# Performance work log

Measured on AMD Instinct MI355X. Metric: run time of the kernel, lower is better.

Reference implementation:

```python
import jax, jax.numpy as jnp
import numpy as np

SEQ_LEN = 12
EMB = 64        # embedding_dim
H = 128         # dec_h_dim
MLP = 1024      # mlp_dim
Z = 32          # z_dim
ZX = MLP + Z    # 1056, width of cat([enc_h_feat, z])
B = 32768


def setup_inputs() -> dict:
    key = jax.random.key(0)
    ks = jax.random.split(key, 16)
    s = 0.05  # weight scale to keep the recurrence stable
    return {
        "last_pos": jax.random.normal(ks[0], (B, 2), jnp.float32),
        "last_pos_rel": jax.random.normal(ks[1], (B, 2), jnp.float32),
        "enc_h_feat": jax.random.normal(ks[2], (B, MLP), jnp.float32),
        "z": jax.random.normal(ks[3], (B, Z), jnp.float32),
        "seq_start_end": jnp.zeros((1, 2), jnp.int64),
        # LSTM params (PyTorch layout: gates ordered i,f,g,o along rows)
        "W_ih": jax.random.normal(ks[4], (4 * H, ZX + EMB), jnp.float32) * s,
        "W_hh": jax.random.normal(ks[5], (4 * H, H), jnp.float32) * s,
        "b_ih": jax.random.normal(ks[6], (4 * H,), jnp.float32) * s,
        "b_hh": jax.random.normal(ks[7], (4 * H,), jnp.float32) * s,
        # mlp: Linear(ZX->MLP), ReLU, Linear(MLP->H), ReLU
        "W1": jax.random.normal(ks[8], (MLP, ZX), jnp.float32) * s,
        "b1": jax.random.normal(ks[9], (MLP,), jnp.float32) * s,
        "W2": jax.random.normal(ks[10], (H, MLP), jnp.float32) * s,
        "b2": jax.random.normal(ks[11], (H,), jnp.float32) * s,
        # spatial_embedding: Linear(2 -> EMB)
        "W_sp": jax.random.normal(ks[12], (EMB, 2), jnp.float32) * s,
        "b_sp": jax.random.normal(ks[13], (EMB,), jnp.float32) * s,
        # hidden2pos: Linear(H -> 2)
        "W_hp": jax.random.normal(ks[14], (2, H), jnp.float32) * s,
        "b_hp": jax.random.normal(ks[15], (2,), jnp.float32) * s,
    }


def _decode(last_pos, last_pos_rel, enc_h_feat, z,
            W_ih, W_hh, b_ih, b_hh, W1, b1, W2, b2, W_sp, b_sp, W_hp, b_hp):
    # initial decoder input from last relative position
    dec_inp = last_pos_rel @ W_sp.T + b_sp                     # [B, EMB]
    zx = jnp.concatenate([enc_h_feat, z], axis=1)              # [B, ZX]
    h = jax.nn.relu(jax.nn.relu(zx @ W1.T + b1) @ W2.T + b2)   # [B, H]
    c = jnp.zeros_like(h)
    # zx is constant across steps: precompute its gate contribution + biases
    W_zx, W_emb = W_ih[:, :ZX], W_ih[:, ZX:]
    zx_proj = zx @ W_zx.T + b_ih + b_hh                        # [B, 4H]

    def step(carry, _):
        h, c, last_pos, dec_inp = carry
        gates = zx_proj + dec_inp @ W_emb.T + h @ W_hh.T       # [B, 4H]
        i, f, g, o = jnp.split(gates, 4, axis=1)
        c = jax.nn.sigmoid(f) * c + jax.nn.sigmoid(i) * jnp.tanh(g)
        h = jax.nn.sigmoid(o) * jnp.tanh(c)
        rel_pos = h @ W_hp.T + b_hp                            # [B, 2]
        last_pos = rel_pos + last_pos
        dec_inp = rel_pos @ W_sp.T + b_sp
        return (h, c, last_pos, dec_inp), rel_pos

    _, pred = jax.lax.scan(step, (h, c, last_pos, dec_inp), None, length=SEQ_LEN)
    return pred  # [SEQ_LEN, B, 2]


def reference(last_pos, last_pos_rel, enc_h_feat, z, seq_start_end,
              W_ih, W_hh, b_ih, b_hh, W1, b1, W2, b2, W_sp, b_sp, W_hp, b_hp):
    # seq_start_end is unused by the original forward
    return _decode(last_pos, last_pos_rel, enc_h_feat, z,
                   W_ih, W_hh, b_ih, b_hh, W1, b1, W2, b2, W_sp, b_sp, W_hp, b_hp)
```

## Files before the change

kernel.cpp:

```cpp
#include <hip/hip_runtime.h>

#define BATCH   32768
#define SEQLEN  12
#define EMB     64
#define H       128
#define MLP     1024
#define Z       32
#define ZX      1056
#define KP      1088
#define NG      512

typedef _Float16 f16x8 __attribute__((ext_vector_type(8)));
typedef float    f32x4 __attribute__((ext_vector_type(4)));

#define S_WCAT_OFF   0u
#define S_W2H_OFF    3244032u
#define S_WHHF_OFF   3506176u
#define S_WC_OFF     3637248u
#define S_BIAS2_OFF  3641344u
#define S_T1_OFF     3643392u
#define S_GP_OFF     70752256u
#define S_H0_OFF     137861120u
#define B_WCAT_OFF   0u
#define B_W2H_OFF    3342336u
#define B_WHHF_OFF   3604480u
#define B_WC_OFF     3735552u
#define B_BIAS2_OFF  3739648u
#define B_T1_OFF     3741696u
#define B_GP_OFF     70850560u
#define B_H0_OFF     137959424u
#define B_ZX16_OFF   146348032u
#define B_TOTAL      217651200ull

__device__ __forceinline__ float sigf(float x) {
    return __builtin_amdgcn_rcpf(1.0f + __expf(-x));
}
__device__ __forceinline__ float tanhfast(float x) {
    return 2.0f * __builtin_amdgcn_rcpf(1.0f + __expf(-2.0f * x)) - 1.0f;
}

__device__ __forceinline__ void gload16(const void* g, void* l) {
    __builtin_amdgcn_global_load_lds(
        (const __attribute__((address_space(1))) unsigned int*)(unsigned long long)(uintptr_t)g,
        (__attribute__((address_space(3))) unsigned int*)(unsigned int)(uintptr_t)l,
        16, 0, 0);
}

__global__ __launch_bounds__(256) void prep_kernel(
    const float* __restrict__ W_ih, const float* __restrict__ W_hh_in,
    const float* __restrict__ b_ih, const float* __restrict__ b_hh,
    const float* __restrict__ W1,   const float* __restrict__ W2,
    const float* __restrict__ W_sp, const float* __restrict__ b_sp,
    const float* __restrict__ W_hp, int cs,
    _Float16* __restrict__ wcat, _Float16* __restrict__ w2h,
    _Float16* __restrict__ whhf, float* __restrict__ wc, float* __restrict__ bias2)
{
    const int bid = blockIdx.x;
    const int tid = threadIdx.x;
    if (bid < 1536) {
        const float* src = (bid < 1024) ? (W1 + (size_t)bid * ZX)
                                        : (W_ih + (size_t)(bid - 1024) * 1120);
        _Float16* dst = wcat + (size_t)bid * cs;
        for (int k = tid; k < cs; k += 256)
            dst[k] = (k < ZX) ? (_Float16)src[k] : (_Float16)0.f;
    } else if (bid < 1664) {
        const int n = bid - 1536;
        for (int k = tid; k < MLP; k += 256)
            w2h[n * MLP + k] = (_Float16)W2[n * MLP + k];
    } else if (bid < 1920) {
        const int n = (bid - 1664) * 2 + (tid >> 7);
        const int k = tid & 127;
        float wc0 = 0.f, wc1 = 0.f;
        for (int e = 0; e < EMB; ++e) {
            const float we = W_ih[(size_t)n * 1120 + ZX + e];
            wc0 += we * W_sp[e * 2];
            wc1 += we * W_sp[e * 2 + 1];
        }
        whhf[n * H + k] = (_Float16)(W_hh_in[n * H + k] + wc0 * W_hp[k] + wc1 * W_hp[H + k]);
    } else {
        const int t = (bid - 1920) * 256 + tid;
        if (t < 1024) {
            const int n = t >> 1, j = t & 1;
            float s = 0.f;
            for (int e = 0; e < EMB; ++e)
                s += W_ih[(size_t)n * 1120 + ZX + e] * W_sp[e * 2 + j];
            wc[t] = s;
        } else if (t < 1536) {
            const int n = t - 1024;
            float s = b_ih[n] + b_hh[n];
            for (int e = 0; e < EMB; ++e)
                s += W_ih[(size_t)n * 1120 + ZX + e] * b_sp[e];
            bias2[n] = s;
        }
    }
}

__global__ __launch_bounds__(256) void zxcast_kernel(
    const float* __restrict__ enc, const float* __restrict__ zin,
    _Float16* __restrict__ zx16)
{
    const int gid = blockIdx.x * 256 + threadIdx.x;
    if (gid < 4194304) {
        const int row = gid >> 7, cw = gid & 127;
        const float4* s = (const float4*)(enc + (size_t)row * MLP + cw * 8);
        const float4 f0 = s[0], f1 = s[1];
        f16x8 v = {(_Float16)f0.x, (_Float16)f0.y, (_Float16)f0.z, (_Float16)f0.w,
                   (_Float16)f1.x, (_Float16)f1.y, (_Float16)f1.z, (_Float16)f1.w};
        *(f16x8*)(zx16 + (size_t)row * KP + cw * 8) = v;
    } else if (gid < 4325376) {
        const int g2 = gid - 4194304;
        const int row = g2 >> 2, cw = g2 & 3;
        const float4* s = (const float4*)(zin + (size_t)row * Z + cw * 8);
        const float4 f0 = s[0], f1 = s[1];
        f16x8 v = {(_Float16)f0.x, (_Float16)f0.y, (_Float16)f0.z, (_Float16)f0.w,
                   (_Float16)f1.x, (_Float16)f1.y, (_Float16)f1.z, (_Float16)f1.w};
        *(f16x8*)(zx16 + (size_t)row * KP + MLP + cw * 8) = v;
    } else {
        const int g2 = gid - 4325376;
        const int row = g2 >> 2, cw = g2 & 3;
        f16x8 v = {};
        *(f16x8*)(zx16 + (size_t)row * KP + ZX + cw * 8) = v;
    }
}

__global__ __launch_bounds__(512, 2) void gemm1_big_kernel(
    const _Float16* __restrict__ zx16, const _Float16* __restrict__ wcat,
    const float* __restrict__ bias1, const float* __restrict__ bias2g,
    _Float16* __restrict__ t1, float* __restrict__ gperm)
{
    __shared__ _Float16 s_a[2][256 * 64];
    __shared__ _Float16 s_b[2][256 * 64];

    const int tid = threadIdx.x;
    const int b   = blockIdx.x;
    const int swz = (b & 7) * 96 + (b >> 3);
    const int mt  = swz / 6, nt = swz % 6;
    const int m0  = mt * 256, n0 = nt * 256;

    const int lane = tid & 63, wv = tid >> 6;
    const int wm   = wv >> 2,  wn = wv & 3;
    const int l15  = lane & 15, q = lane >> 4;

    const int rowS = tid >> 3;
    const int chS  = (tid & 7) ^ (rowS & 7);

    const _Float16* gA = zx16 + (size_t)(m0 + rowS) * KP + chS * 8;
    const _Float16* gB = wcat + (size_t)(n0 + rowS) * KP + chS * 8;
    const size_t rstep = (size_t)64 * KP;

    const int ph0  = q ^ (l15 & 7);
    const int ph1  = (4 + q) ^ (l15 & 7);
    const int aof0 = (wm * 128 + l15) * 64 + ph0 * 8;
    const int aof1 = (wm * 128 + l15) * 64 + ph1 * 8;
    const int bof0 = (wn * 64 + l15) * 64 + ph0 * 8;
    const int bof1 = (wn * 64 + l15) * 64 + ph1 * 8;

    f32x4 acc[8][4] = {};

    {
        _Float16* dA = &s_a[0][0] + wv * 512;
        _Float16* dB = &s_b[0][0] + wv * 512;
        #pragma unroll
        for (int j = 0; j < 4; ++j) gload16(gA + j * rstep, dA + j * 4096);
        #pragma unroll
        for (int j = 0; j < 4; ++j) gload16(gB + j * rstep, dB + j * 4096);
    }

    #pragma unroll 2
    for (int kt = 0; kt < 16; ++kt) {
        const int cur = kt & 1;
        const _Float16* sA = &s_a[cur][0];
        const _Float16* sB = &s_b[cur][0];
        _Float16* dA = &s_a[cur ^ 1][0] + wv * 512;
        _Float16* dB = &s_b[cur ^ 1][0] + wv * 512;
        const _Float16* gA1 = gA + (kt + 1) * 64;
        const _Float16* gB1 = gB + (kt + 1) * 64;

        f16x8 af[4], bf[4];

        gload16(gA1,         dA);
        gload16(gA1 + rstep, dA + 4096);
        asm volatile("s_waitcnt vmcnt(2)\n\ts_barrier" ::: "memory");
        #pragma unroll
        for (int i = 0; i < 4; ++i) af[i] = *(const f16x8*)(sA + aof0 + i * 1024);
        #pragma unroll
        for (int i = 0; i < 4; ++i) bf[i] = *(const f16x8*)(sB + bof0 + i * 1024);
        __builtin_amdgcn_s_setprio(1);
        #pragma unroll
        for (int n_ = 0; n_ < 4; ++n_)
            #pragma unroll
            for (int m_ = 0; m_ < 4; ++m_)
                acc[m_][n_] = __builtin_amdgcn_mfma_f32_16x16x32_f16(af[m_], bf[n_], acc[m_][n_], 0, 0, 0);
        __builtin_amdgcn_s_setprio(0);
        asm volatile("s_barrier" ::: "memory");

        gload16(gA1 + 2 * rstep, dA + 8192);
        gload16(gA1 + 3 * rstep, dA + 12288);
        #pragma unroll
        for (int i = 0; i < 4; ++i) af[i] = *(const f16x8*)(sA + aof0 + 4096 + i * 1024);
        asm volatile("s_barrier" ::: "memory");
        __builtin_amdgcn_s_setprio(1);
        #pragma unroll
        for (int n_ = 0; n_ < 4; ++n_)
            #pragma unroll
            for (int m_ = 0; m_ < 4; ++m_)
                acc[4 + m_][n_] = __builtin_amdgcn_mfma_f32_16x16x32_f16(af[m_], bf[n_], acc[4 + m_][n_], 0, 0, 0);
        __builtin_amdgcn_s_setprio(0);
        asm volatile("s_barrier" ::: "memory");

        gload16(gB1,         dB);
        gload16(gB1 + rstep, dB + 4096);
        #pragma unroll
        for (int i = 0; i < 4; ++i) af[i] = *(const f16x8*)(sA + aof1 + i * 1024);
        #pragma unroll
        for (int i = 0; i < 4; ++i) bf[i] = *(const f16x8*)(sB + bof1 + i * 1024);
        asm volatile("s_barrier" ::: "memory");
        __builtin_amdgcn_s_setprio(1);
        #pragma unroll
        for (int n_ = 0; n_ < 4; ++n_)
            #pragma unroll
            for (int m_ = 0; m_ < 4; ++m_)
                acc[m_][n_] = __builtin_amdgcn_mfma_f32_16x16x32_f16(af[m_], bf[n_], acc[m_][n_], 0, 0, 0);
        __builtin_amdgcn_s_setprio(0);
        asm volatile("s_barrier" ::: "memory");

        gload16(gB1 + 2 * rstep, dB + 8192);
        gload16(gB1 + 3 * rstep, dB + 12288);
        #pragma unroll
        for (int i = 0; i < 4; ++i) af[i] = *(const f16x8*)(sA + aof1 + 4096 + i * 1024);
        asm volatile("s_barrier" ::: "memory");
        __builtin_amdgcn_s_setprio(1);
        #pragma unroll
        for (int n_ = 0; n_ < 4; ++n_)
            #pragma unroll
            for (int m_ = 0; m_ < 4; ++m_)
                acc[4 + m_][n_] = __builtin_amdgcn_mfma_f32_16x16x32_f16(af[m_], bf[n_], acc[4 + m_][n_], 0, 0, 0);
        __builtin_amdgcn_s_setprio(0);
        asm volatile("s_barrier" ::: "memory");
    }

    {
        const _Float16* sA = &s_a[0][0];
        const _Float16* sB = &s_b[0][0];
        asm volatile("s_waitcnt vmcnt(0)\n\ts_barrier" ::: "memory");
        f16x8 af[4], bf[4];
        #pragma unroll
        for (int i = 0; i < 4; ++i) af[i] = *(const f16x8*)(sA + aof0 + i * 1024);
        #pragma unroll
        for (int i = 0; i < 4; ++i) bf[i] = *(const f16x8*)(sB + bof0 + i * 1024);
        __builtin_amdgcn_s_setprio(1);
        #pragma unroll
        for (int n_ = 0; n_ < 4; ++n_)
            #pragma unroll
            for (int m_ = 0; m_ < 4; ++m_)
                acc[m_][n_] = __builtin_amdgcn_mfma_f32_16x16x32_f16(af[m_], bf[n_], acc[m_][n_], 0, 0, 0);
        #pragma unroll
        for (int i = 0; i < 4; ++i) af[i] = *(const f16x8*)(sA + aof0 + 4096 + i * 1024);
        #pragma unroll
        for (int n_ = 0; n_ < 4; ++n_)
            #pragma unroll
            for (int m_ = 0; m_ < 4; ++m_)
                acc[4 + m_][n_] = __builtin_amdgcn_mfma_f32_16x16x32_f16(af[m_], bf[n_], acc[4 + m_][n_], 0, 0, 0);
        #pragma unroll
        for (int i = 0; i < 4; ++i) af[i] = *(const f16x8*)(sA + aof1 + i * 1024);
        #pragma unroll
        for (int i = 0; i < 4; ++i) bf[i] = *(const f16x8*)(sB + bof1 + i * 1024);
        #pragma unroll
        for (int n_ = 0; n_ < 4; ++n_)
            #pragma unroll
            for (int m_ = 0; m_ < 4; ++m_)
                acc[m_][n_] = __builtin_amdgcn_mfma_f32_16x16x32_f16(af[m_], bf[n_], acc[m_][n_], 0, 0, 0);
        #pragma unroll
        for (int i = 0; i < 4; ++i) af[i] = *(const f16x8*)(sA + aof1 + 4096 + i * 1024);
        #pragma unroll
        for (int n_ = 0; n_ < 4; ++n_)
            #pragma unroll
            for (int m_ = 0; m_ < 4; ++m_)
                acc[4 + m_][n_] = __builtin_amdgcn_mfma_f32_16x16x32_f16(af[m_], bf[n_], acc[4 + m_][n_], 0, 0, 0);
        __builtin_amdgcn_s_setprio(0);
    }

    if (nt < 4) {
        #pragma unroll
        for (int im = 0; im < 8; ++im)
            #pragma unroll
            for (int in_ = 0; in_ < 4; ++in_) {
                const int n = n0 + wn * 64 + in_ * 16 + l15;
                const float bb = bias1[n];
                const int mbase = m0 + wm * 128 + im * 16 + q * 4;
                #pragma unroll
                for (int r = 0; r < 4; ++r) {
                    float v = acc[im][in_][r] + bb;
                    v = v > 0.f ? v : 0.f;
                    t1[(size_t)(mbase + r) * MLP + n] = (_Float16)v;
                }
            }
    } else {
        #pragma unroll
        for (int im = 0; im < 8; ++im)
            #pragma unroll
            for (int in_ = 0; in_ < 4; ++in_) {
                const int n = (n0 - 1024) + wn * 64 + in_ * 16 + l15;
                const float bb = bias2g[n];
                const int m4 = (m0 + wm * 128 + im * 16 + q * 4) >> 2;
                float4 v;
                v.x = acc[im][in_][0] + bb;
                v.y = acc[im][in_][1] + bb;
                v.z = acc[im][in_][2] + bb;
                v.w = acc[im][in_][3] + bb;
                *(float4*)(gperm + ((size_t)m4 * NG + n) * 4) = v;
            }
    }
}

__global__ __launch_bounds__(256) void gemm1_small_kernel(
    const float* __restrict__ enc, const float* __restrict__ zin,
    const _Float16* __restrict__ wcat,
    const float* __restrict__ bias1, const float* __restrict__ bias2g,
    _Float16* __restrict__ t1, float* __restrict__ gperm)
{
    __shared__ float    s_a[128 * 32];
    __shared__ _Float16 s_b[128 * 32];

    const int tid = threadIdx.x;
    const int b = blockIdx.x;
    const int x = b & 7, s = b >> 3;
    const int mt = x * 32 + s / 12;
    const int bn = s % 12;
    const int m0 = mt * 128;

    const int lane = tid & 63, wv = tid >> 6;
    const int wm = wv >> 1, wn = wv & 1;
    const int l15 = lane & 15, q = lane >> 4;

    const int rowA = tid >> 3;
    const int chA  = (tid & 7) ^ ((tid >> 3) & 7);
    const int rowB = tid >> 2;
    const int chB  = (tid & 3) ^ ((tid >> 3) & 3);

    const int ca0 = (2 * q) ^ (l15 & 7);
    const int cb  = q ^ ((l15 >> 1) & 3);

    f32x4 acc[4][4] = {};

    for (int kt = 0; kt < 33; ++kt) {
        const float* abase;
        size_t astride;
        if (kt < 32) { abase = enc + (size_t)m0 * MLP + kt * 32; astride = MLP; }
        else         { abase = zin + (size_t)m0 * Z;             astride = Z;   }

        __syncthreads();
        #pragma unroll
        for (int i = 0; i < 4; ++i)
            gload16(abase + (size_t)(i * 32 + rowA) * astride + chA * 4,
                    s_a + i * 1024 + wv * 256);
        #pragma unroll
        for (int i = 0; i < 2; ++i)
            gload16(wcat + (size_t)(bn * 128 + i * 64 + rowB) * ZX + kt * 32 + chB * 8,
                    s_b + i * 2048 + wv * 512);
        __syncthreads();

        f16x8 af[4];
        #pragma unroll
        for (int im = 0; im < 4; ++im) {
            const float* ap = s_a + (wm * 64 + im * 16 + l15) * 32;
            const float4 f0 = *(const float4*)(ap + ca0 * 4);
            const float4 f1 = *(const float4*)(ap + (ca0 ^ 1) * 4);
            af[im] = f16x8{(_Float16)f0.x, (_Float16)f0.y, (_Float16)f0.z, (_Float16)f0.w,
                           (_Float16)f1.x, (_Float16)f1.y, (_Float16)f1.z, (_Float16)f1.w};
        }
        #pragma unroll
        for (int in_ = 0; in_ < 4; ++in_) {
            const f16x8 bf = *(const f16x8*)(s_b + (wn * 64 + in_ * 16 + l15) * 32 + cb * 8);
            #pragma unroll
            for (int im = 0; im < 4; ++im)
                acc[im][in_] = __builtin_amdgcn_mfma_f32_16x16x32_f16(af[im], bf, acc[im][in_], 0, 0, 0);
        }
    }

    if (bn < 8) {
        #pragma unroll
        for (int im = 0; im < 4; ++im)
            #pragma unroll
            for (int in_ = 0; in_ < 4; ++in_) {
                const int n = bn * 128 + wn * 64 + in_ * 16 + l15;
                const float bb = bias1[n];
                #pragma unroll
                for (int r = 0; r < 4; ++r) {
                    const int m = m0 + wm * 64 + im * 16 + q * 4 + r;
                    float v = acc[im][in_][r] + bb;
                    v = v > 0.f ? v : 0.f;
                    t1[(size_t)m * MLP + n] = (_Float16)v;
                }
            }
    } else {
        #pragma unroll
        for (int im = 0; im < 4; ++im)
            #pragma unroll
            for (int in_ = 0; in_ < 4; ++in_) {
                const int n = (bn - 8) * 128 + wn * 64 + in_ * 16 + l15;
                const float bb = bias2g[n];
                const int m4 = (m0 + wm * 64 + im * 16 + q * 4) >> 2;
                float4 v;
                v.x = acc[im][in_][0] + bb;
                v.y = acc[im][in_][1] + bb;
                v.z = acc[im][in_][2] + bb;
                v.w = acc[im][in_][3] + bb;
                *(float4*)(gperm + ((size_t)m4 * NG + n) * 4) = v;
            }
    }
}

__global__ __launch_bounds__(256) void gemm2_kernel(
    const _Float16* __restrict__ t1, const _Float16* __restrict__ w2h,
    const float* __restrict__ b2, _Float16* __restrict__ h0buf)
{
    __shared__ _Float16 s_a[64 * 32];
    __shared__ _Float16 s_b[128 * 32];

    const int tid = threadIdx.x;
    const int m0  = blockIdx.x * 64;
    const int lane = tid & 63, wv = tid >> 6;
    const int l15 = lane & 15, q = lane >> 4;

    const int rowS = tid >> 2;
    const int chS  = ((tid & 3) ^ (tid >> 2) ^ (tid >> 4)) & 3;
    const int phF  = (q ^ l15 ^ (l15 >> 2)) & 3;

    f32x4 acc[4][2] = {};

    for (int kt = 0; kt < 32; ++kt) {
        __syncthreads();
        gload16(t1 + (size_t)(m0 + rowS) * MLP + kt * 32 + chS * 8,
                s_a + wv * 512);
        #pragma unroll
        for (int i = 0; i < 2; ++i) {
            const int row = i * 64 + rowS;
            const int c   = ((tid & 3) ^ row ^ (row >> 2)) & 3;
            gload16(w2h + (size_t)row * MLP + kt * 32 + c * 8,
                    s_b + i * 2048 + wv * 512);
        }
        __syncthreads();

        f16x8 af[4];
        #pragma unroll
        for (int im = 0; im < 4; ++im)
            af[im] = *(const f16x8*)(s_a + (im * 16 + l15) * 32 + phF * 8);
        #pragma unroll
        for (int in_ = 0; in_ < 2; ++in_) {
            const f16x8 bf = *(const f16x8*)(s_b + (wv * 32 + in_ * 16 + l15) * 32 + phF * 8);
            #pragma unroll
            for (int im = 0; im < 4; ++im)
                acc[im][in_] = __builtin_amdgcn_mfma_f32_16x16x32_f16(af[im], bf, acc[im][in_], 0, 0, 0);
        }
    }

    #pragma unroll
    for (int im = 0; im < 4; ++im)
        #pragma unroll
        for (int in_ = 0; in_ < 2; ++in_) {
            const int n = wv * 32 + in_ * 16 + l15;
            const float bb = b2[n];
            #pragma unroll
            for (int r = 0; r < 4; ++r) {
                const int m = m0 + im * 16 + q * 4 + r;
                float v = acc[im][in_][r] + bb;
                v = v > 0.f ? v : 0.f;
                h0buf[(size_t)m * H + n] = (_Float16)v;
            }
        }
}

__global__ __launch_bounds__(512) void recur_kernel(
    const float* __restrict__ gperm, const _Float16* __restrict__ h0buf,
    const _Float16* __restrict__ whhf, const float* __restrict__ wc,
    const float* __restrict__ whp, const float* __restrict__ bhp,
    const float* __restrict__ lpr, float* __restrict__ out)
{
    __shared__ _Float16 s_whh[512 * 136];
    __shared__ _Float16 s_h[64 * 136];
    __shared__ float    s_p[128];
    __shared__ float    s_wc[1024];
    __shared__ float    s_whp[256];
    __shared__ float    s_bhp[2];

    const int tid = threadIdx.x;
    const int m0  = blockIdx.x * 64;
    const int lane = tid & 63, w = tid >> 6;
    const int l15 = lane & 15, q = lane >> 4;

    #pragma unroll
    for (int i = 0; i < 16; ++i) {
        const int cid = tid + i * 512;
        const int row = cid >> 4, ch = cid & 15;
        *(uint4*)(s_whh + row * 136 + ch * 8) = *(const uint4*)(whhf + row * H + ch * 8);
    }
    if (tid < 256) *(float4*)(s_wc + tid * 4)  = *(const float4*)(wc + tid * 4);
    if (tid < 64)  *(float4*)(s_whp + tid * 4) = *(const float4*)(whp + tid * 4);
    if (tid < 2)   s_bhp[tid] = bhp[tid];
    if (tid < 128) s_p[tid] = lpr[(size_t)m0 * 2 + tid];
    {
        const int row = tid >> 3, ch = tid & 7;
        *(uint4*)(s_h + row * 136 + ch * 16)     = *(const uint4*)(h0buf + (size_t)(m0 + row) * H + ch * 16);
        *(uint4*)(s_h + row * 136 + ch * 16 + 8) = *(const uint4*)(h0buf + (size_t)(m0 + row) * H + ch * 16 + 8);
    }

    f32x4 gb[4][4];
    #pragma unroll
    for (int im = 0; im < 4; ++im) {
        const int m4 = (m0 >> 2) + im * 4 + q;
        #pragma unroll
        for (int g = 0; g < 4; ++g) {
            const float4 v = *(const float4*)(gperm + ((size_t)m4 * NG + g * H + w * 16 + l15) * 4);
            gb[im][g] = f32x4{v.x, v.y, v.z, v.w};
        }
    }

    f32x4 cst[4] = {};

    __syncthreads();

    {
        const int part = tid & 3;
        const int j    = (tid >> 2) & 1;
        const int row  = tid >> 3;
        float sum = 0.f;
        #pragma unroll
        for (int u = 0; u < 4; ++u) {
            const f16x8 hv = *(const f16x8*)(s_h + row * 136 + part * 32 + u * 8);
            const float4* wp = (const float4*)(s_whp + j * H + part * 32 + u * 8);
            const float4 w0 = wp[0], w1 = wp[1];
            sum += (float)hv[0] * w0.x + (float)hv[1] * w0.y + (float)hv[2] * w0.z + (float)hv[3] * w0.w
                 + (float)hv[4] * w1.x + (float)hv[5] * w1.y + (float)hv[6] * w1.z + (float)hv[7] * w1.w;
        }
        sum += __shfl_down(sum, 2, 64);
        sum += __shfl_down(sum, 1, 64);
        if (part == 0) s_p[row * 2 + j] -= sum;
    }
    __syncthreads();

    float wc0[4], wc1[4], cg[4];
    #pragma unroll
    for (int g = 0; g < 4; ++g) {
        const int n = g * H + w * 16 + l15;
        wc0[g] = s_wc[n * 2];
        wc1[g] = s_wc[n * 2 + 1];
        cg[g]  = wc0[g] * s_bhp[0] + wc1[g] * s_bhp[1];
    }
    #pragma unroll
    for (int im = 0; im < 4; ++im)
        #pragma unroll
        for (int r = 0; r < 4; ++r) {
            const int mrow = im * 16 + q * 4 + r;
            const float pa = s_p[mrow * 2], pb = s_p[mrow * 2 + 1];
            #pragma unroll
            for (int g = 0; g < 4; ++g)
                gb[im][g][r] += pa * wc0[g] + pb * wc1[g];
        }

    for (int t = 0; t < SEQLEN; ++t) {
        f32x4 acc[4][4];
        #pragma unroll
        for (int kt = 0; kt < 4; ++kt) {
            f16x8 af[4];
            #pragma unroll
            for (int im = 0; im < 4; ++im)
                af[im] = *(const f16x8*)(s_h + (im * 16 + l15) * 136 + kt * 32 + q * 8);
            #pragma unroll
            for (int g = 0; g < 4; ++g) {
                const f16x8 bf = *(const f16x8*)(s_whh + (g * H + w * 16 + l15) * 136 + kt * 32 + q * 8);
                #pragma unroll
                for (int im = 0; im < 4; ++im)
                    acc[im][g] = __builtin_amdgcn_mfma_f32_16x16x32_f16(
                        af[im], bf, (kt == 0) ? gb[im][g] : acc[im][g], 0, 0, 0);
            }
        }
        __syncthreads();

        #pragma unroll
        for (int im = 0; im < 4; ++im) {
            #pragma unroll
            for (int r = 0; r < 4; ++r) {
                const int mrow = im * 16 + q * 4 + r;
                const float cc = sigf(acc[im][1][r]) * cst[im][r]
                               + sigf(acc[im][0][r]) * tanhfast(acc[im][2][r]);
                cst[im][r] = cc;
                const float hh = sigf(acc[im][3][r]) * tanhfast(cc);
                s_h[mrow * 136 + w * 16 + l15] = (_Float16)hh;
            }
        }
        if (t == 0) {
            #pragma unroll
            for (int im = 0; im < 4; ++im)
                #pragma unroll
                for (int r = 0; r < 4; ++r) {
                    const int mrow = im * 16 + q * 4 + r;
                    const float pa = s_p[mrow * 2], pb = s_p[mrow * 2 + 1];
                    #pragma unroll
                    for (int g = 0; g < 4; ++g)
                        gb[im][g][r] += cg[g] - (pa * wc0[g] + pb * wc1[g]);
                }
        }
        __syncthreads();

        {
            const int part = tid & 3;
            const int j    = (tid >> 2) & 1;
            const int row  = tid >> 3;
            float sum = 0.f;
            #pragma unroll
            for (int u = 0; u < 4; ++u) {
                const f16x8 hv = *(const f16x8*)(s_h + row * 136 + part * 32 + u * 8);
                const float4* wp = (const float4*)(s_whp + j * H + part * 32 + u * 8);
                const float4 w0 = wp[0], w1 = wp[1];
                sum += (float)hv[0] * w0.x + (float)hv[1] * w0.y + (float)hv[2] * w0.z + (float)hv[3] * w0.w
                     + (float)hv[4] * w1.x + (float)hv[5] * w1.y + (float)hv[6] * w1.z + (float)hv[7] * w1.w;
            }
            sum += __shfl_down(sum, 2, 64);
            sum += __shfl_down(sum, 1, 64);
            if (part == 0)
                out[(size_t)t * (BATCH * 2) + (size_t)(m0 + row) * 2 + j] = sum + s_bhp[j];
        }
    }
}

extern "C" void kernel_launch(void* const* d_in, const int* in_sizes, int n_in,
                              void* d_out, int out_size, void* d_ws, size_t ws_size,
                              hipStream_t stream)
{
    const float* last_pos_rel = (const float*)d_in[1];
    const float* enc          = (const float*)d_in[2];
    const float* zin          = (const float*)d_in[3];
    const float* W_ih         = (const float*)d_in[5];
    const float* W_hh         = (const float*)d_in[6];
    const float* b_ih         = (const float*)d_in[7];
    const float* b_hh         = (const float*)d_in[8];
    const float* W1           = (const float*)d_in[9];
    const float* b1           = (const float*)d_in[10];
    const float* W2           = (const float*)d_in[11];
    const float* b2           = (const float*)d_in[12];
    const float* W_sp         = (const float*)d_in[13];
    const float* b_sp         = (const float*)d_in[14];
    const float* W_hp         = (const float*)d_in[15];
    const float* b_hp         = (const float*)d_in[16];
    float* out = (float*)d_out;

    char* ws = (char*)d_ws;
    const bool big = (ws_size >= B_TOTAL);

    _Float16* wcat  = (_Float16*)(ws + (big ? B_WCAT_OFF  : S_WCAT_OFF));
    _Float16* w2h   = (_Float16*)(ws + (big ? B_W2H_OFF   : S_W2H_OFF));
    _Float16* whhf  = (_Float16*)(ws + (big ? B_WHHF_OFF  : S_WHHF_OFF));
    float*    wc    = (float*)(ws + (big ? B_WC_OFF    : S_WC_OFF));
    float*    bias2 = (float*)(ws + (big ? B_BIAS2_OFF : S_BIAS2_OFF));
    _Float16* t1    = (_Float16*)(ws + (big ? B_T1_OFF : S_T1_OFF));
    float*    gperm = (float*)(ws + (big ? B_GP_OFF : S_GP_OFF));
    _Float16* h0b   = (_Float16*)(ws + (big ? B_H0_OFF : S_H0_OFF));
    _Float16* zx16  = (_Float16*)(ws + B_ZX16_OFF);

    prep_kernel<<<dim3(1926), 256, 0, stream>>>(W_ih, W_hh, b_ih, b_hh, W1, W2, W_sp, b_sp,
                                                W_hp, big ? KP : ZX, wcat, w2h, whhf, wc, bias2);
    if (big) {
        zxcast_kernel<<<dim3(17408), 256, 0, stream>>>(enc, zin, zx16);
        gemm1_big_kernel<<<dim3(768), 512, 0, stream>>>(zx16, wcat, b1, bias2, t1, gperm);
    } else {
        gemm1_small_kernel<<<dim3(3072), 256, 0, stream>>>(enc, zin, wcat, b1, bias2, t1, gperm);
    }
    gemm2_kernel<<<dim3(512), 256, 0, stream>>>(t1, w2h, b2, h0b);
    recur_kernel<<<dim3(512), 512, 0, stream>>>(gperm, h0b, whhf, wc, W_hp, b_hp,
                                                last_pos_rel, out);
}
```

Before: 482.7 us.

## Keep W_hh fragments in registers and overlap output projection with MFMA

The recurrent kernel no longer stages the W_hh gate weights (about 139 KB) in shared memory. Each wave now loads its B-fragments once into registers, which frees LDS and, with launch_bounds(512,2), is meant to let two blocks share a CU. The hidden2pos projection for step t-1 is moved to just after the step-t MFMAs, before the barrier, which removes one __syncthreads per step; a final projection runs after the loop. s_whp is padded to a 36-float stride to cut LDS bank conflicts. The cost is 64 extra VGPRs per thread under a tighter register cap, which could cause spills.

```diff
diff --git a/kernel.cpp b/kernel.cpp
--- a/kernel.cpp
+++ b/kernel.cpp
@@ -471,17 +471,16 @@
         }
 }
 
-__global__ __launch_bounds__(512) void recur_kernel(
+__global__ __launch_bounds__(512, 2) void recur_kernel(
     const float* __restrict__ gperm, const _Float16* __restrict__ h0buf,
     const _Float16* __restrict__ whhf, const float* __restrict__ wc,
     const float* __restrict__ whp, const float* __restrict__ bhp,
     const float* __restrict__ lpr, float* __restrict__ out)
 {
-    __shared__ _Float16 s_whh[512 * 136];
     __shared__ _Float16 s_h[64 * 136];
     __shared__ float    s_p[128];
     __shared__ float    s_wc[1024];
-    __shared__ float    s_whp[256];
+    __shared__ float    s_whp[8 * 36];
     __shared__ float    s_bhp[2];
 
     const int tid = threadIdx.x;
@@ -489,14 +488,20 @@
     const int lane = tid & 63, w = tid >> 6;
     const int l15 = lane & 15, q = lane >> 4;
 
+    f16x8 bfr[4][4];
     #pragma unroll
-    for (int i = 0; i < 16; ++i) {
-        const int cid = tid + i * 512;
-        const int row = cid >> 4, ch = cid & 15;
-        *(uint4*)(s_whh + row * 136 + ch * 8) = *(const uint4*)(whhf + row * H + ch * 8);
-    }
+    for (int g = 0; g < 4; ++g)
+        #pragma unroll
+        for (int kt = 0; kt < 4; ++kt)
+            bfr[g][kt] = *(const f16x8*)(whhf + (size_t)(g * H + w * 16 + l15) * H + kt * 32 + q * 8);
+
     if (tid < 256) *(float4*)(s_wc + tid * 4)  = *(const float4*)(wc + tid * 4);
-    if (tid < 64)  *(float4*)(s_whp + tid * 4) = *(const float4*)(whp + tid * 4);
+    if (tid < 64) {
+        const int jp = tid >> 3;
+        const int e8 = tid & 7;
+        const int j = jp >> 2, part = jp & 3;
+        *(float4*)(s_whp + jp * 36 + e8 * 4) = *(const float4*)(whp + j * H + part * 32 + e8 * 4);
+    }
     if (tid < 2)   s_bhp[tid] = bhp[tid];
     if (tid < 128) s_p[tid] = lpr[(size_t)m0 * 2 + tid];
     {
@@ -524,11 +529,12 @@
         const int part = tid & 3;
         const int j    = (tid >> 2) & 1;
         const int row  = tid >> 3;
+        const int jp   = j * 4 + part;
         float sum = 0.f;
         #pragma unroll
         for (int u = 0; u < 4; ++u) {
             const f16x8 hv = *(const f16x8*)(s_h + row * 136 + part * 32 + u * 8);
-            const float4* wp = (const float4*)(s_whp + j * H + part * 32 + u * 8);
+            const float4* wp = (const float4*)(s_whp + jp * 36 + u * 8);
             const float4 w0 = wp[0], w1 = wp[1];
             sum += (float)hv[0] * w0.x + (float)hv[1] * w0.y + (float)hv[2] * w0.z + (float)hv[3] * w0.w
                  + (float)hv[4] * w1.x + (float)hv[5] * w1.y + (float)hv[6] * w1.z + (float)hv[7] * w1.w;
@@ -568,12 +574,30 @@
                 af[im] = *(const f16x8*)(s_h + (im * 16 + l15) * 136 + kt * 32 + q * 8);
             #pragma unroll
             for (int g = 0; g < 4; ++g) {
-                const f16x8 bf = *(const f16x8*)(s_whh + (g * H + w * 16 + l15) * 136 + kt * 32 + q * 8);
                 #pragma unroll
                 for (int im = 0; im < 4; ++im)
                     acc[im][g] = __builtin_amdgcn_mfma_f32_16x16x32_f16(
-                        af[im], bf, (kt == 0) ? gb[im][g] : acc[im][g], 0, 0, 0);
-            }
+                        af[im], bfr[g][kt], (kt == 0) ? gb[im][g] : acc[im][g], 0, 0, 0);
+            }
+        }
+        if (t > 0) {
+            const int part = tid & 3;
+            const int j    = (tid >> 2) & 1;
+            const int row  = tid >> 3;
+            const int jp   = j * 4 + part;
+            float sum = 0.f;
+            #pragma unroll
+            for (int u = 0; u < 4; ++u) {
+                const f16x8 hv = *(const f16x8*)(s_h + row * 136 + part * 32 + u * 8);
+                const float4* wp = (const float4*)(s_whp + jp * 36 + u * 8);
+                const float4 w0 = wp[0], w1 = wp[1];
+                sum += (float)hv[0] * w0.x + (float)hv[1] * w0.y + (float)hv[2] * w0.z + (float)hv[3] * w0.w
+                     + (float)hv[4] * w1.x + (float)hv[5] * w1.y + (float)hv[6] * w1.z + (float)hv[7] * w1.w;
+            }
+            sum += __shfl_down(sum, 2, 64);
+            sum += __shfl_down(sum, 1, 64);
+            if (part == 0)
+                out[(size_t)(t - 1) * (BATCH * 2) + (size_t)(m0 + row) * 2 + j] = sum + s_bhp[j];
         }
         __syncthreads();
 
@@ -602,25 +626,26 @@
                 }
         }
         __syncthreads();
-
-        {
-            const int part = tid & 3;
-            const int j    = (tid >> 2) & 1;
-            const int row  = tid >> 3;
-            float sum = 0.f;
-            #pragma unroll
-            for (int u = 0; u < 4; ++u) {
-                const f16x8 hv = *(const f16x8*)(s_h + row * 136 + part * 32 + u * 8);
-                const float4* wp = (const float4*)(s_whp + j * H + part * 32 + u * 8);
-                const float4 w0 = wp[0], w1 = wp[1];
-                sum += (float)hv[0] * w0.x + (float)hv[1] * w0.y + (float)hv[2] * w0.z + (float)hv[3] * w0.w
-                     + (float)hv[4] * w1.x + (float)hv[5] * w1.y + (float)hv[6] * w1.z + (float)hv[7] * w1.w;
-            }
-            sum += __shfl_down(sum, 2, 64);
-            sum += __shfl_down(sum, 1, 64);
-            if (part == 0)
-                out[(size_t)t * (BATCH * 2) + (size_t)(m0 + row) * 2 + j] = sum + s_bhp[j];
-        }
+    }
+
+    {
+        const int part = tid & 3;
+        const int j    = (tid >> 2) & 1;
+        const int row  = tid >> 3;
+        const int jp   = j * 4 + part;
+        float sum = 0.f;
+        #pragma unroll
+        for (int u = 0; u < 4; ++u) {
+            const f16x8 hv = *(const f16x8*)(s_h + row * 136 + part * 32 + u * 8);
+            const float4* wp = (const float4*)(s_whp + jp * 36 + u * 8);
+            const float4 w0 = wp[0], w1 = wp[1];
+            sum += (float)hv[0] * w0.x + (float)hv[1] * w0.y + (float)hv[2] * w0.z + (float)hv[3] * w0.w
+                 + (float)hv[4] * w1.x + (float)hv[5] * w1.y + (float)hv[6] * w1.z + (float)hv[7] * w1.w;
+        }
+        sum += __shfl_down(sum, 2, 64);
+        sum += __shfl_down(sum, 1, 64);
+        if (part == 0)
+            out[(size_t)(SEQLEN - 1) * (BATCH * 2) + (size_t)(m0 + row) * 2 + j] = sum + s_bhp[j];
     }
 }
 
```

Measured after the change: 560.8 us. 16.2% more time.

## Software-pipeline LSTM recurrence by splitting row tile into two halves

Applied to the files above, without the earlier changes.

The 64-row tile in the recurrent kernel is split into two 32-row halves. The MFMA gate computation for one half is interleaved with the LSTM cell update and hidden-to-position reduction for the other half, so matrix-core work can overlap with transcendental and LDS work across the barriers. The hidden2pos reduction is also restructured to use 8 lanes per output, reading a padded shared weight layout. In exchange, control flow gets more complex, with a prologue MFMA and an epilogue output write, and two sets of accumulators raise register pressure.

```diff
diff --git a/kernel.cpp b/kernel.cpp
--- a/kernel.cpp
+++ b/kernel.cpp
@@ -471,6 +471,54 @@
         }
 }
 
+__device__ __forceinline__ float relpos16(const _Float16* s_h, const float* s_whp,
+                                          int row, int j, int p) {
+    const f16x8 a = *(const f16x8*)(s_h + row * 136 + p * 16);
+    const f16x8 b = *(const f16x8*)(s_h + row * 136 + p * 16 + 8);
+    const float* wp = s_whp + (j * 4 + (p >> 1)) * 36 + (p & 1) * 16;
+    float s = 0.f;
+    #pragma unroll
+    for (int u = 0; u < 8; ++u)
+        s += (float)a[u] * wp[u] + (float)b[u] * wp[8 + u];
+    s += __shfl_down(s, 4, 64);
+    s += __shfl_down(s, 2, 64);
+    s += __shfl_down(s, 1, 64);
+    return s;
+}
+
+#define MFMA_H(x, ACC)                                                              \
+    {                                                                               \
+        _Pragma("unroll")                                                           \
+        for (int kt = 0; kt < 4; ++kt) {                                            \
+            const f16x8 af0 = *(const f16x8*)(s_h + ((x) * 32 + l15) * 136 + kt * 32 + q * 8); \
+            const f16x8 af1 = *(const f16x8*)(s_h + ((x) * 32 + 16 + l15) * 136 + kt * 32 + q * 8); \
+            _Pragma("unroll")                                                       \
+            for (int g = 0; g < 4; ++g) {                                           \
+                const f16x8 bf = *(const f16x8*)(s_whh + (g * H + w * 16 + l15) * 136 + kt * 32 + q * 8); \
+                ACC[0][g] = __builtin_amdgcn_mfma_f32_16x16x32_f16(af0, bf,         \
+                    (kt == 0) ? gb[(x) * 2][g] : ACC[0][g], 0, 0, 0);               \
+                ACC[1][g] = __builtin_amdgcn_mfma_f32_16x16x32_f16(af1, bf,         \
+                    (kt == 0) ? gb[(x) * 2 + 1][g] : ACC[1][g], 0, 0, 0);           \
+            }                                                                       \
+        }                                                                           \
+    }
+
+#define CELL_H(x, ACC)                                                              \
+    {                                                                               \
+        _Pragma("unroll")                                                           \
+        for (int im2 = 0; im2 < 2; ++im2) {                                         \
+            _Pragma("unroll")                                                       \
+            for (int r = 0; r < 4; ++r) {                                           \
+                const int mrow = (x) * 32 + im2 * 16 + q * 4 + r;                   \
+                const float cc = sigf(ACC[im2][1][r]) * cst[(x) * 2 + im2][r]       \
+                               + sigf(ACC[im2][0][r]) * tanhfast(ACC[im2][2][r]);   \
+                cst[(x) * 2 + im2][r] = cc;                                         \
+                const float hh = sigf(ACC[im2][3][r]) * tanhfast(cc);               \
+                s_h[mrow * 136 + w * 16 + l15] = (_Float16)hh;                      \
+            }                                                                       \
+        }                                                                           \
+    }
+
 __global__ __launch_bounds__(512) void recur_kernel(
     const float* __restrict__ gperm, const _Float16* __restrict__ h0buf,
     const _Float16* __restrict__ whhf, const float* __restrict__ wc,
@@ -481,7 +529,7 @@
     __shared__ _Float16 s_h[64 * 136];
     __shared__ float    s_p[128];
     __shared__ float    s_wc[1024];
-    __shared__ float    s_whp[256];
+    __shared__ float    s_whp[8 * 36];
     __shared__ float    s_bhp[2];
 
     const int tid = threadIdx.x;
@@ -496,7 +544,12 @@
         *(uint4*)(s_whh + row * 136 + ch * 8) = *(const uint4*)(whhf + row * H + ch * 8);
     }
     if (tid < 256) *(float4*)(s_wc + tid * 4)  = *(const float4*)(wc + tid * 4);
-    if (tid < 64)  *(float4*)(s_whp + tid * 4) = *(const float4*)(whp + tid * 4);
+    if (tid < 64) {
+        const int jp = tid >> 3;
+        const int e8 = tid & 7;
+        const int j = jp >> 2, part = jp & 3;
+        *(float4*)(s_whp + jp * 36 + e8 * 4) = *(const float4*)(whp + j * H + part * 32 + e8 * 4);
+    }
     if (tid < 2)   s_bhp[tid] = bhp[tid];
     if (tid < 128) s_p[tid] = lpr[(size_t)m0 * 2 + tid];
     {
@@ -524,11 +577,12 @@
         const int part = tid & 3;
         const int j    = (tid >> 2) & 1;
         const int row  = tid >> 3;
+        const int jp   = j * 4 + part;
         float sum = 0.f;
         #pragma unroll
         for (int u = 0; u < 4; ++u) {
             const f16x8 hv = *(const f16x8*)(s_h + row * 136 + part * 32 + u * 8);
-            const float4* wp = (const float4*)(s_whp + j * H + part * 32 + u * 8);
+            const float4* wp = (const float4*)(s_whp + jp * 36 + u * 8);
             const float4 w0 = wp[0], w1 = wp[1];
             sum += (float)hv[0] * w0.x + (float)hv[1] * w0.y + (float)hv[2] * w0.z + (float)hv[3] * w0.w
                  + (float)hv[4] * w1.x + (float)hv[5] * w1.y + (float)hv[6] * w1.z + (float)hv[7] * w1.w;
@@ -558,37 +612,15 @@
                 gb[im][g][r] += pa * wc0[g] + pb * wc1[g];
         }
 
+    const int rp_p = tid & 7, rp_j = (tid >> 3) & 1, rp_r = tid >> 4;
+
+    f32x4 accE[2][4], accO[2][4];
+
+    MFMA_H(0, accE);
+    __syncthreads();
+
     for (int t = 0; t < SEQLEN; ++t) {
-        f32x4 acc[4][4];
-        #pragma unroll
-        for (int kt = 0; kt < 4; ++kt) {
-            f16x8 af[4];
-            #pragma unroll
-            for (int im = 0; im < 4; ++im)
-                af[im] = *(const f16x8*)(s_h + (im * 16 + l15) * 136 + kt * 32 + q * 8);
-            #pragma unroll
-            for (int g = 0; g < 4; ++g) {
-                const f16x8 bf = *(const f16x8*)(s_whh + (g * H + w * 16 + l15) * 136 + kt * 32 + q * 8);
-                #pragma unroll
-                for (int im = 0; im < 4; ++im)
-                    acc[im][g] = __builtin_amdgcn_mfma_f32_16x16x32_f16(
-                        af[im], bf, (kt == 0) ? gb[im][g] : acc[im][g], 0, 0, 0);
-            }
-        }
-        __syncthreads();
-
-        #pragma unroll
-        for (int im = 0; im < 4; ++im) {
-            #pragma unroll
-            for (int r = 0; r < 4; ++r) {
-                const int mrow = im * 16 + q * 4 + r;
-                const float cc = sigf(acc[im][1][r]) * cst[im][r]
-                               + sigf(acc[im][0][r]) * tanhfast(acc[im][2][r]);
-                cst[im][r] = cc;
-                const float hh = sigf(acc[im][3][r]) * tanhfast(cc);
-                s_h[mrow * 136 + w * 16 + l15] = (_Float16)hh;
-            }
-        }
+        MFMA_H(1, accO);
         if (t == 0) {
             #pragma unroll
             for (int im = 0; im < 4; ++im)
@@ -600,27 +632,32 @@
                     for (int g = 0; g < 4; ++g)
                         gb[im][g][r] += cg[g] - (pa * wc0[g] + pb * wc1[g]);
                 }
-        }
+        } else {
+            const float sm = relpos16(s_h, s_whp, 32 + rp_r, rp_j, rp_p);
+            if (rp_p == 0)
+                out[(size_t)(t - 1) * (BATCH * 2) + (size_t)(m0 + 32 + rp_r) * 2 + rp_j]
+                    = sm + s_bhp[rp_j];
+        }
+        CELL_H(0, accE);
         __syncthreads();
 
+        if (t < SEQLEN - 1)
+            MFMA_H(0, accE);
         {
-            const int part = tid & 3;
-            const int j    = (tid >> 2) & 1;
-            const int row  = tid >> 3;
-            float sum = 0.f;
-            #pragma unroll
-            for (int u = 0; u < 4; ++u) {
-                const f16x8 hv = *(const f16x8*)(s_h + row * 136 + part * 32 + u * 8);
-                const float4* wp = (const float4*)(s_whp + j * H + part * 32 + u * 8);
-                const float4 w0 = wp[0], w1 = wp[1];
-                sum += (float)hv[0] * w0.x + (float)hv[1] * w0.y + (float)hv[2] * w0.z + (float)hv[3] * w0.w
-                     + (float)hv[4] * w1.x + (float)hv[5] * w1.y + (float)hv[6] * w1.z + (float)hv[7] * w1.w;
-            }
-            sum += __shfl_down(sum, 2, 64);
-            sum += __shfl_down(sum, 1, 64);
-            if (part == 0)
-                out[(size_t)t * (BATCH * 2) + (size_t)(m0 + row) * 2 + j] = sum + s_bhp[j];
-        }
+            const float sm = relpos16(s_h, s_whp, rp_r, rp_j, rp_p);
+            if (rp_p == 0)
+                out[(size_t)t * (BATCH * 2) + (size_t)(m0 + rp_r) * 2 + rp_j]
+                    = sm + s_bhp[rp_j];
+        }
+        CELL_H(1, accO);
+        __syncthreads();
+    }
+
+    {
+        const float sm = relpos16(s_h, s_whp, 32 + rp_r, rp_j, rp_p);
+        if (rp_p == 0)
+            out[(size_t)(SEQLEN - 1) * (BATCH * 2) + (size_t)(m0 + 32 + rp_r) * 2 + rp_j]
+                = sm + s_bhp[rp_j];
     }
 }
 
```

Result: slower. 503.0 us (+4.2%).

## Double recurrence block threads and overlap hidden-to-pos projection with MFMA phase

Applied to the files above, without the earlier changes.

The recurrence kernel now launches 1024 threads per block, splitting the 64 rows across two wave groups so each wave holds half as many accumulators. The hidden-to-position reduction for step t-1 is moved into the slot between the MFMA phase and the barrier of step t, which removes one barrier per step, and a final projection is done after the loop. The W_hp layout in shared memory is padded to lower bank conflicts. This raises register pressure limits through launch bounds and may reduce blocks per CU given the large shared-memory footprint.

```diff
diff --git a/kernel.cpp b/kernel.cpp
--- a/kernel.cpp
+++ b/kernel.cpp
@@ -471,7 +471,22 @@
         }
 }
 
-__global__ __launch_bounds__(512) void recur_kernel(
+__device__ __forceinline__ float relpos16(const _Float16* s_h, const float* s_whp,
+                                          int row, int j, int p) {
+    const f16x8 a = *(const f16x8*)(s_h + row * 136 + p * 16);
+    const f16x8 b = *(const f16x8*)(s_h + row * 136 + p * 16 + 8);
+    const float* wp = s_whp + (j * 4 + (p >> 1)) * 36 + (p & 1) * 16;
+    float s = 0.f;
+    #pragma unroll
+    for (int u = 0; u < 8; ++u)
+        s += (float)a[u] * wp[u] + (float)b[u] * wp[8 + u];
+    s += __shfl_down(s, 4, 64);
+    s += __shfl_down(s, 2, 64);
+    s += __shfl_down(s, 1, 64);
+    return s;
+}
+
+__global__ __launch_bounds__(1024, 4) void recur_kernel(
     const float* __restrict__ gperm, const _Float16* __restrict__ h0buf,
     const _Float16* __restrict__ whhf, const float* __restrict__ wc,
     const float* __restrict__ whp, const float* __restrict__ bhp,
@@ -481,54 +496,62 @@
     __shared__ _Float16 s_h[64 * 136];
     __shared__ float    s_p[128];
     __shared__ float    s_wc[1024];
-    __shared__ float    s_whp[256];
+    __shared__ float    s_whp[8 * 36];
     __shared__ float    s_bhp[2];
 
     const int tid = threadIdx.x;
     const int m0  = blockIdx.x * 64;
-    const int lane = tid & 63, w = tid >> 6;
+    const int lane = tid & 63;
+    const int w16 = tid >> 6;
+    const int wg  = w16 & 7;
+    const int wm2 = w16 >> 3;
     const int l15 = lane & 15, q = lane >> 4;
 
     #pragma unroll
-    for (int i = 0; i < 16; ++i) {
-        const int cid = tid + i * 512;
+    for (int i = 0; i < 8; ++i) {
+        const int cid = tid + i * 1024;
         const int row = cid >> 4, ch = cid & 15;
         *(uint4*)(s_whh + row * 136 + ch * 8) = *(const uint4*)(whhf + row * H + ch * 8);
     }
     if (tid < 256) *(float4*)(s_wc + tid * 4)  = *(const float4*)(wc + tid * 4);
-    if (tid < 64)  *(float4*)(s_whp + tid * 4) = *(const float4*)(whp + tid * 4);
+    if (tid < 64) {
+        const int jp = tid >> 3;
+        const int e8 = tid & 7;
+        const int j = jp >> 2, part = jp & 3;
+        *(float4*)(s_whp + jp * 36 + e8 * 4) = *(const float4*)(whp + j * H + part * 32 + e8 * 4);
+    }
     if (tid < 2)   s_bhp[tid] = bhp[tid];
     if (tid < 128) s_p[tid] = lpr[(size_t)m0 * 2 + tid];
     {
-        const int row = tid >> 3, ch = tid & 7;
-        *(uint4*)(s_h + row * 136 + ch * 16)     = *(const uint4*)(h0buf + (size_t)(m0 + row) * H + ch * 16);
-        *(uint4*)(s_h + row * 136 + ch * 16 + 8) = *(const uint4*)(h0buf + (size_t)(m0 + row) * H + ch * 16 + 8);
-    }
-
-    f32x4 gb[4][4];
+        const int row = tid >> 4, ch = tid & 15;
+        *(uint4*)(s_h + row * 136 + ch * 8) = *(const uint4*)(h0buf + (size_t)(m0 + row) * H + ch * 8);
+    }
+
+    f32x4 gb[2][4];
     #pragma unroll
-    for (int im = 0; im < 4; ++im) {
-        const int m4 = (m0 >> 2) + im * 4 + q;
+    for (int im = 0; im < 2; ++im) {
+        const int m4 = (m0 >> 2) + wm2 * 8 + im * 4 + q;
         #pragma unroll
         for (int g = 0; g < 4; ++g) {
-            const float4 v = *(const float4*)(gperm + ((size_t)m4 * NG + g * H + w * 16 + l15) * 4);
+            const float4 v = *(const float4*)(gperm + ((size_t)m4 * NG + g * H + wg * 16 + l15) * 4);
             gb[im][g] = f32x4{v.x, v.y, v.z, v.w};
         }
     }
 
-    f32x4 cst[4] = {};
+    f32x4 cst[2] = {};
 
     __syncthreads();
 
-    {
+    if (tid < 512) {
         const int part = tid & 3;
         const int j    = (tid >> 2) & 1;
         const int row  = tid >> 3;
+        const int jp   = j * 4 + part;
         float sum = 0.f;
         #pragma unroll
         for (int u = 0; u < 4; ++u) {
             const f16x8 hv = *(const f16x8*)(s_h + row * 136 + part * 32 + u * 8);
-            const float4* wp = (const float4*)(s_whp + j * H + part * 32 + u * 8);
+            const float4* wp = (const float4*)(s_whp + jp * 36 + u * 8);
             const float4 w0 = wp[0], w1 = wp[1];
             sum += (float)hv[0] * w0.x + (float)hv[1] * w0.y + (float)hv[2] * w0.z + (float)hv[3] * w0.w
                  + (float)hv[4] * w1.x + (float)hv[5] * w1.y + (float)hv[6] * w1.z + (float)hv[7] * w1.w;
@@ -542,59 +565,52 @@
     float wc0[4], wc1[4], cg[4];
     #pragma unroll
     for (int g = 0; g < 4; ++g) {
-        const int n = g * H + w * 16 + l15;
+        const int n = g * H + wg * 16 + l15;
         wc0[g] = s_wc[n * 2];
         wc1[g] = s_wc[n * 2 + 1];
         cg[g]  = wc0[g] * s_bhp[0] + wc1[g] * s_bhp[1];
     }
     #pragma unroll
-    for (int im = 0; im < 4; ++im)
+    for (int im = 0; im < 2; ++im)
         #pragma unroll
         for (int r = 0; r < 4; ++r) {
-            const int mrow = im * 16 + q * 4 + r;
+            const int mrow = wm2 * 32 + im * 16 + q * 4 + r;
             const float pa = s_p[mrow * 2], pb = s_p[mrow * 2 + 1];
             #pragma unroll
             for (int g = 0; g < 4; ++g)
                 gb[im][g][r] += pa * wc0[g] + pb * wc1[g];
         }
 
+    const int rp_p = tid & 7, rp_j = (tid >> 3) & 1, rp_r = tid >> 4;
+
     for (int t = 0; t < SEQLEN; ++t) {
-        f32x4 acc[4][4];
+        f32x4 acc[2][4];
         #pragma unroll
         for (int kt = 0; kt < 4; ++kt) {
-            f16x8 af[4];
-            #pragma unroll
-            for (int im = 0; im < 4; ++im)
-                af[im] = *(const f16x8*)(s_h + (im * 16 + l15) * 136 + kt * 32 + q * 8);
+            f16x8 af[2];
+            #pragma unroll
+            for (int im = 0; im < 2; ++im)
+                af[im] = *(const f16x8*)(s_h + (wm2 * 32 + im * 16 + l15) * 136 + kt * 32 + q * 8);
             #pragma unroll
             for (int g = 0; g < 4; ++g) {
-                const f16x8 bf = *(const f16x8*)(s_whh + (g * H + w * 16 + l15) * 136 + kt * 32 + q * 8);
+                const f16x8 bf = *(const f16x8*)(s_whh + (g * H + wg * 16 + l15) * 136 + kt * 32 + q * 8);
                 #pragma unroll
-                for (int im = 0; im < 4; ++im)
+                for (int im = 0; im < 2; ++im)
                     acc[im][g] = __builtin_amdgcn_mfma_f32_16x16x32_f16(
                         af[im], bf, (kt == 0) ? gb[im][g] : acc[im][g], 0, 0, 0);
             }
         }
-        __syncthreads();
-
-        #pragma unroll
-        for (int im = 0; im < 4; ++im) {
-            #pragma unroll
-            for (int r = 0; r < 4; ++r) {
-                const int mrow = im * 16 + q * 4 + r;
-                const float cc = sigf(acc[im][1][r]) * cst[im][r]
-                               + sigf(acc[im][0][r]) * tanhfast(acc[im][2][r]);
-                cst[im][r] = cc;
-                const float hh = sigf(acc[im][3][r]) * tanhfast(cc);
-                s_h[mrow * 136 + w * 16 + l15] = (_Float16)hh;
-            }
-        }
-        if (t == 0) {
-            #pragma unroll
-            for (int im = 0; im < 4; ++im)
+        if (t > 0) {
+            const float sm = relpos16(s_h, s_whp, rp_r, rp_j, rp_p);
+            if (rp_p == 0)
+                out[(size_t)(t - 1) * (BATCH * 2) + (size_t)(m0 + rp_r) * 2 + rp_j]
+                    = sm + s_bhp[rp_j];
+        } else {
+            #pragma unroll
+            for (int im = 0; im < 2; ++im)
                 #pragma unroll
                 for (int r = 0; r < 4; ++r) {
-                    const int mrow = im * 16 + q * 4 + r;
+                    const int mrow = wm2 * 32 + im * 16 + q * 4 + r;
                     const float pa = s_p[mrow * 2], pb = s_p[mrow * 2 + 1];
                     #pragma unroll
                     for (int g = 0; g < 4; ++g)
@@ -603,24 +619,26 @@
         }
         __syncthreads();
 
-        {
-            const int part = tid & 3;
-            const int j    = (tid >> 2) & 1;
-            const int row  = tid >> 3;
-            float sum = 0.f;
-            #pragma unroll
-            for (int u = 0; u < 4; ++u) {
-                const f16x8 hv = *(const f16x8*)(s_h + row * 136 + part * 32 + u * 8);
-                const float4* wp = (const float4*)(s_whp + j * H + part * 32 + u * 8);
-                const float4 w0 = wp[0], w1 = wp[1];
-                sum += (float)hv[0] * w0.x + (float)hv[1] * w0.y + (float)hv[2] * w0.z + (float)hv[3] * w0.w
-                     + (float)hv[4] * w1.x + (float)hv[5] * w1.y + (float)hv[6] * w1.z + (float)hv[7] * w1.w;
+        #pragma unroll
+        for (int im = 0; im < 2; ++im) {
+            #pragma unroll
+            for (int r = 0; r < 4; ++r) {
+                const int mrow = wm2 * 32 + im * 16 + q * 4 + r;
+                const float cc = sigf(acc[im][1][r]) * cst[im][r]
+                               + sigf(acc[im][0][r]) * tanhfast(acc[im][2][r]);
+                cst[im][r] = cc;
+                const float hh = sigf(acc[im][3][r]) * tanhfast(cc);
+                s_h[mrow * 136 + wg * 16 + l15] = (_Float16)hh;
             }
-            sum += __shfl_down(sum, 2, 64);
-            sum += __shfl_down(sum, 1, 64);
-            if (part == 0)
-                out[(size_t)t * (BATCH * 2) + (size_t)(m0 + row) * 2 + j] = sum + s_bhp[j];
-        }
+        }
+        __syncthreads();
+    }
+
+    {
+        const float sm = relpos16(s_h, s_whp, rp_r, rp_j, rp_p);
+        if (rp_p == 0)
+            out[(size_t)(SEQLEN - 1) * (BATCH * 2) + (size_t)(m0 + rp_r) * 2 + rp_j]
+                = sm + s_bhp[rp_j];
     }
 }
 
@@ -667,6 +685,6 @@
         gemm1_small_kernel<<<dim3(3072), 256, 0, stream>>>(enc, zin, wcat, b1, bias2, t1, gperm);
     }
     gemm2_kernel<<<dim3(512), 256, 0, stream>>>(t1, w2h, b2, h0b);
-    recur_kernel<<<dim3(512), 512, 0, stream>>>(gperm, h0b, whhf, wc, W_hp, b_hp,
-                                                last_pos_rel, out);
-}
+    recur_kernel<<<dim3(512), 1024, 0, stream>>>(gperm, h0b, whhf, wc, W_hp, b_hp,
+                                                 last_pos_rel, out);
+}
```

After: 531.8 us. +10.2%, slower.
